# Kernel tuning notes

Hardware: AMD Instinct MI355X
Metric: run time of the kernel (lower is better)

Reference implementation:

```python
import jax, jax.numpy as jnp
import numpy as np

USER_NUM = 100000
ITEM_NUM = 100000
DIM = 64
BS = 256


def setup_inputs() -> dict:
    key = jax.random.key(0)
    k1, k2, k3, k4, k5 = jax.random.split(key, 5)
    # xavier_normal-ish scale for embeddings/linear
    user_table = jax.random.normal(k1, (USER_NUM, DIM), dtype=jnp.float32) * 0.1
    item_table = jax.random.normal(k2, (ITEM_NUM, DIM), dtype=jnp.float32) * 0.1
    cls_w = jax.random.normal(k3, (5, DIM), dtype=jnp.float32) * (2.0 / (DIM + 5)) ** 0.5
    cls_b = jnp.zeros((5,), dtype=jnp.float32)
    batch_user = jax.random.randint(k4, (BS,), 0, USER_NUM, dtype=jnp.int64)
    values = jnp.array([[1.0, 2.0, 3.0, 4.0, 5.0]], dtype=jnp.float32)
    return {
        "batch_user": batch_user,
        "user_table": user_table,
        "item_table": item_table,
        "cls_w": cls_w,
        "cls_b": cls_b,
        "values": values,
    }


def reference(batch_user, user_table, item_table, cls_w, cls_b, values):
    # forward_full_items: score every (user, item) pair.
    # Torch materializes h_ui = (u repeated) * (items tiled) of shape
    # [bs*item_num, dim]; mathematically logits = einsum over dim, so we
    # fuse the broadcasted product with the tiny Linear to avoid the
    # huge expanded intermediate while computing identical math.
    u = user_table[batch_user]                       # [bs, dim]
    # logits[b,i,c] = sum_d u[b,d] * item[i,d] * W[c,d] + b[c]
    logits = jnp.einsum('bd,id,cd->bic', u, item_table, cls_w) + cls_b  # [bs, item_num, 5]
    prob = jax.nn.softmax(logits, axis=-1)
    return jnp.sum(prob * values[0], axis=-1)        # [bs, item_num]
```

## Files before the change

### kernel.cpp

```cpp
#include <hip/hip_runtime.h>

#define I_TOTAL 100000
#define DIM 64
#define BS 256

typedef __attribute__((ext_vector_type(8))) short bf16x8;
typedef __attribute__((ext_vector_type(4))) float f32x4;

__device__ inline unsigned short f2bf(float x) {
    union { float f; unsigned u; } v; v.f = x;
    return (unsigned short)((v.u + 0x8000u) >> 16);
}

__global__ __launch_bounds__(256) void prep_M(
    const int* __restrict__ bu, const float* __restrict__ ut,
    const float* __restrict__ cw, unsigned short* __restrict__ Mbf)
{
    int idx = blockIdx.x * 256 + threadIdx.x;
    int d = (idx & 15) * 4;
    int n = idx >> 4;
    int c = n >> 8, b = n & 255;
    const float s = 1.4426950408889634f;
    float4 u = *(const float4*)(ut + (long)bu[b] * DIM + d);
    float4 w = *(const float4*)(cw + c * DIM + d);
    ushort4 r;
    r.x = f2bf(u.x * w.x * s);
    r.y = f2bf(u.y * w.y * s);
    r.z = f2bf(u.z * w.z * s);
    r.w = f2bf(u.w * w.w * s);
    *(ushort4*)(Mbf + n * DIM + d) = r;
}

__global__ __launch_bounds__(256) void conv_items(
    const float* __restrict__ item, unsigned short* __restrict__ itbf)
{
    long t = (long)blockIdx.x * 256 + threadIdx.x;
    const float4* p = (const float4*)(item + t * 8);
    float4 a = p[0], b = p[1];
    ushort4 r0, r1;
    r0.x = f2bf(a.x); r0.y = f2bf(a.y); r0.z = f2bf(a.z); r0.w = f2bf(a.w);
    r1.x = f2bf(b.x); r1.y = f2bf(b.y); r1.z = f2bf(b.z); r1.w = f2bf(b.w);
    ushort4* q = (ushort4*)(itbf + t * 8);
    q[0] = r0; q[1] = r1;
}

__global__ __launch_bounds__(256) void gemm_softmax(
    const unsigned short* __restrict__ itbf,
    const unsigned short* __restrict__ Mbf,
    const float* __restrict__ clsb, const float* __restrict__ vals,
    float* __restrict__ out)
{
    __shared__ float ldsb[4224];

    const int blk = blockIdx.x;
    const int r8 = blk & 7;
    const int q  = blk >> 3;
    const int g  = q & 15;
    const int a  = q >> 4;
    const int y  = a * 8 + r8;
    if (y >= 98) return;

    const int lane = threadIdx.x & 63;
    const int wave = threadIdx.x >> 6;
    const int col  = lane & 15;
    const int quad = lane >> 4;

    const int b_base = g * 16;
    const int i_base = y * 1024 + wave * 256;

    bf16x8 afr[5][2];
#pragma unroll
    for (int c = 0; c < 5; ++c) {
        const unsigned short* p = Mbf + (c * BS + b_base + col) * DIM + quad * 8;
        afr[c][0] = *(const bf16x8*)p;
        afr[c][1] = *(const bf16x8*)(p + 32);
    }

    const f32x4 zero = (f32x4){0.f, 0.f, 0.f, 0.f};
    const float s = 1.4426950408889634f;
    float bb[5], vv[5];
#pragma unroll
    for (int c = 0; c < 5; ++c) { bb[c] = clsb[c] * s; vv[c] = vals[c]; }

    if (y < 97) {
        float* wlds = ldsb + wave * 1056 + quad * 264 + col;
        const float* rlds = ldsb + wave * 1056 + quad * 264 + 4 * col;

        float* op[4];
#pragma unroll
        for (int k = 0; k < 4; ++k)
            op[k] = out + (size_t)(b_base + quad * 4 + k) * I_TOTAL + (i_base + 4 * col);

        const unsigned short* bp = itbf + (size_t)(i_base + col) * DIM + quad * 8;

#pragma unroll 1
        for (int t4 = 0; t4 < 4; ++t4) {
#pragma unroll
            for (int ti = 0; ti < 4; ++ti) {
                bf16x8 b0 = *(const bf16x8*)(bp + ti * 1024);
                bf16x8 b1 = *(const bf16x8*)(bp + ti * 1024 + 32);
                f32x4 acc[5];
#pragma unroll
                for (int c = 0; c < 5; ++c) {
                    acc[c] = __builtin_amdgcn_mfma_f32_16x16x32_bf16(afr[c][0], b0, zero, 0, 0, 0);
                    acc[c] = __builtin_amdgcn_mfma_f32_16x16x32_bf16(afr[c][1], b1, acc[c], 0, 0, 0);
                }
                f32x4 l[5];
#pragma unroll
                for (int c = 0; c < 5; ++c) l[c] = acc[c] + bb[c];
#pragma unroll
                for (int rr = 0; rr < 4; ++rr) {
                    float e0 = __builtin_amdgcn_exp2f(l[0][rr]);
                    float e1 = __builtin_amdgcn_exp2f(l[1][rr]);
                    float e2 = __builtin_amdgcn_exp2f(l[2][rr]);
                    float e3 = __builtin_amdgcn_exp2f(l[3][rr]);
                    float e4 = __builtin_amdgcn_exp2f(l[4][rr]);
                    float den = ((e0 + e1) + (e2 + e3)) + e4;
                    float num = e0 * vv[0];
                    num = fmaf(e1, vv[1], num);
                    num = fmaf(e2, vv[2], num);
                    num = fmaf(e3, vv[3], num);
                    num = fmaf(e4, vv[4], num);
                    wlds[rr * 64 + ti * 16] = num * __builtin_amdgcn_rcpf(den);
                }
            }
#pragma unroll
            for (int k = 0; k < 4; ++k) {
                f32x4 o4 = *(const f32x4*)(rlds + k * 64);
                *(f32x4*)op[k] = o4;
                op[k] += 64;
            }
            bp += 4 * 1024;
        }
    } else {
#pragma unroll 1
        for (int t = 0; t < 16; ++t) {
            int i  = i_base + t * 16 + col;
            int ic = i < I_TOTAL ? i : I_TOTAL - 1;
            const unsigned short* p2 = itbf + (size_t)ic * DIM + quad * 8;
            bf16x8 b0 = *(const bf16x8*)p2;
            bf16x8 b1 = *(const bf16x8*)(p2 + 32);
            f32x4 acc[5];
#pragma unroll
            for (int c = 0; c < 5; ++c) {
                acc[c] = __builtin_amdgcn_mfma_f32_16x16x32_bf16(afr[c][0], b0, zero, 0, 0, 0);
                acc[c] = __builtin_amdgcn_mfma_f32_16x16x32_bf16(afr[c][1], b1, acc[c], 0, 0, 0);
            }
            if (i < I_TOTAL) {
#pragma unroll
                for (int rr = 0; rr < 4; ++rr) {
                    float e0 = __builtin_amdgcn_exp2f(acc[0][rr] + bb[0]);
                    float e1 = __builtin_amdgcn_exp2f(acc[1][rr] + bb[1]);
                    float e2 = __builtin_amdgcn_exp2f(acc[2][rr] + bb[2]);
                    float e3 = __builtin_amdgcn_exp2f(acc[3][rr] + bb[3]);
                    float e4 = __builtin_amdgcn_exp2f(acc[4][rr] + bb[4]);
                    float den = ((e0 + e1) + (e2 + e3)) + e4;
                    float num = e0 * vv[0];
                    num = fmaf(e1, vv[1], num);
                    num = fmaf(e2, vv[2], num);
                    num = fmaf(e3, vv[3], num);
                    num = fmaf(e4, vv[4], num);
                    out[(size_t)(b_base + quad * 4 + rr) * I_TOTAL + i] =
                        num * __builtin_amdgcn_rcpf(den);
                }
            }
        }
    }
}

__global__ __launch_bounds__(256) void gemm_softmax_fb(
    const float* __restrict__ item, const unsigned short* __restrict__ Mbf,
    const float* __restrict__ clsb, const float* __restrict__ vals,
    float* __restrict__ out)
{
    const int lane = threadIdx.x & 63;
    const int wave = threadIdx.x >> 6;
    const int col  = lane & 15;
    const int quad = lane >> 4;
    const int  b_base = blockIdx.x * 16;
    const long i_wave = (long)blockIdx.y * 256 + wave * 64;

    bf16x8 afr[5][2];
#pragma unroll
    for (int c = 0; c < 5; ++c) {
        const unsigned short* p = Mbf + (c * BS + b_base + col) * DIM + quad * 8;
        afr[c][0] = *(const bf16x8*)p;
        afr[c][1] = *(const bf16x8*)(p + 32);
    }
    f32x4 acc[5][4];
#pragma unroll
    for (int c = 0; c < 5; ++c)
#pragma unroll
        for (int t = 0; t < 4; ++t) acc[c][t] = (f32x4){0.f,0.f,0.f,0.f};
#pragma unroll
    for (int t = 0; t < 4; ++t) {
        long i  = i_wave + t * 16 + col;
        long ic = (i < I_TOTAL) ? i : (I_TOTAL - 1);
        const float4* fp = (const float4*)(item + ic * DIM);
        float4 q0 = fp[2*quad], q1 = fp[2*quad+1], q2 = fp[8+2*quad], q3 = fp[8+2*quad+1];
        bf16x8 b0, b1;
        b0[0]=(short)f2bf(q0.x); b0[1]=(short)f2bf(q0.y); b0[2]=(short)f2bf(q0.z); b0[3]=(short)f2bf(q0.w);
        b0[4]=(short)f2bf(q1.x); b0[5]=(short)f2bf(q1.y); b0[6]=(short)f2bf(q1.z); b0[7]=(short)f2bf(q1.w);
        b1[0]=(short)f2bf(q2.x); b1[1]=(short)f2bf(q2.y); b1[2]=(short)f2bf(q2.z); b1[3]=(short)f2bf(q2.w);
        b1[4]=(short)f2bf(q3.x); b1[5]=(short)f2bf(q3.y); b1[6]=(short)f2bf(q3.z); b1[7]=(short)f2bf(q3.w);
#pragma unroll
        for (int c = 0; c < 5; ++c) {
            acc[c][t] = __builtin_amdgcn_mfma_f32_16x16x32_bf16(afr[c][0], b0, acc[c][t], 0, 0, 0);
            acc[c][t] = __builtin_amdgcn_mfma_f32_16x16x32_bf16(afr[c][1], b1, acc[c][t], 0, 0, 0);
        }
    }
    const float s = 1.4426950408889634f;
    float bb[5], vv[5];
#pragma unroll
    for (int c = 0; c < 5; ++c) { bb[c] = clsb[c] * s; vv[c] = vals[c]; }
#pragma unroll
    for (int t = 0; t < 4; ++t) {
        long i = i_wave + t * 16 + col;
        if (i >= I_TOTAL) continue;
#pragma unroll
        for (int r = 0; r < 4; ++r) {
            int b = b_base + quad * 4 + r;
            float num = 0.f, den = 0.f;
#pragma unroll
            for (int c = 0; c < 5; ++c) {
                float e = __builtin_amdgcn_exp2f(acc[c][t][r] + bb[c]);
                den += e; num = fmaf(e, vv[c], num);
            }
            out[(long)b * I_TOTAL + i] = num * __builtin_amdgcn_rcpf(den);
        }
    }
}

extern "C" void kernel_launch(void* const* d_in, const int* in_sizes, int n_in,
                              void* d_out, int out_size, void* d_ws, size_t ws_size,
                              hipStream_t stream) {
    const int*   bu   = (const int*)d_in[0];
    const float* ut   = (const float*)d_in[1];
    const float* it   = (const float*)d_in[2];
    const float* cw   = (const float*)d_in[3];
    const float* cb   = (const float*)d_in[4];
    const float* vals = (const float*)d_in[5];
    float* out = (float*)d_out;
    unsigned short* Mbf  = (unsigned short*)d_ws;
    unsigned short* itbf = (unsigned short*)((char*)d_ws + 163840);

    const size_t needed = 163840 + (size_t)I_TOTAL * DIM * 2;

    prep_M<<<80, 256, 0, stream>>>(bu, ut, cw, Mbf);
    if (ws_size >= needed) {
        conv_items<<<3125, 256, 0, stream>>>(it, itbf);
        gemm_softmax<<<1664, 256, 0, stream>>>(itbf, Mbf, cb, vals, out);
    } else {
        dim3 grid(16, 391);
        gemm_softmax_fb<<<grid, 256, 0, stream>>>(it, Mbf, cb, vals, out);
    }
}
```

Baseline: 177.7 us.

## Software-pipeline item-tile loads against MFMA and softmax, use nontemporal stores

After: 184.6 us. 3.9% more time.

```diff
diff --git a/kernel.cpp b/kernel.cpp
--- a/kernel.cpp
+++ b/kernel.cpp
@@ -93,44 +93,100 @@
 
         const unsigned short* bp = itbf + (size_t)(i_base + col) * DIM + quad * 8;
 
+        bf16x8 ra0 = *(const bf16x8*)(bp);
+        bf16x8 ra1 = *(const bf16x8*)(bp + 32);
+        bf16x8 ra2 = *(const bf16x8*)(bp + 1024);
+        bf16x8 ra3 = *(const bf16x8*)(bp + 1024 + 32);
+
 #pragma unroll 1
-        for (int t4 = 0; t4 < 4; ++t4) {
-#pragma unroll
-            for (int ti = 0; ti < 4; ++ti) {
-                bf16x8 b0 = *(const bf16x8*)(bp + ti * 1024);
-                bf16x8 b1 = *(const bf16x8*)(bp + ti * 1024 + 32);
-                f32x4 acc[5];
-#pragma unroll
-                for (int c = 0; c < 5; ++c) {
-                    acc[c] = __builtin_amdgcn_mfma_f32_16x16x32_bf16(afr[c][0], b0, zero, 0, 0, 0);
-                    acc[c] = __builtin_amdgcn_mfma_f32_16x16x32_bf16(afr[c][1], b1, acc[c], 0, 0, 0);
+        for (int q4 = 0; q4 < 4; ++q4) {
+            f32x4 accA[2][5];
+#pragma unroll
+            for (int c = 0; c < 5; ++c) {
+                accA[0][c] = __builtin_amdgcn_mfma_f32_16x16x32_bf16(afr[c][0], ra0, zero, 0, 0, 0);
+                accA[0][c] = __builtin_amdgcn_mfma_f32_16x16x32_bf16(afr[c][1], ra1, accA[0][c], 0, 0, 0);
+                accA[1][c] = __builtin_amdgcn_mfma_f32_16x16x32_bf16(afr[c][0], ra2, zero, 0, 0, 0);
+                accA[1][c] = __builtin_amdgcn_mfma_f32_16x16x32_bf16(afr[c][1], ra3, accA[1][c], 0, 0, 0);
+            }
+            bf16x8 rb0 = *(const bf16x8*)(bp + 2048);
+            bf16x8 rb1 = *(const bf16x8*)(bp + 2048 + 32);
+            bf16x8 rb2 = *(const bf16x8*)(bp + 3072);
+            bf16x8 rb3 = *(const bf16x8*)(bp + 3072 + 32);
+
+#pragma unroll
+            for (int t = 0; t < 2; ++t) {
+                f32x4 l0 = accA[t][0] + bb[0];
+                f32x4 l1 = accA[t][1] + bb[1];
+                f32x4 l2 = accA[t][2] + bb[2];
+                f32x4 l3 = accA[t][3] + bb[3];
+                f32x4 l4 = accA[t][4] + bb[4];
+                f32x4 e0, e1, e2, e3, e4;
+#pragma unroll
+                for (int j = 0; j < 4; ++j) {
+                    e0[j] = __builtin_amdgcn_exp2f(l0[j]);
+                    e1[j] = __builtin_amdgcn_exp2f(l1[j]);
+                    e2[j] = __builtin_amdgcn_exp2f(l2[j]);
+                    e3[j] = __builtin_amdgcn_exp2f(l3[j]);
+                    e4[j] = __builtin_amdgcn_exp2f(l4[j]);
                 }
-                f32x4 l[5];
-#pragma unroll
-                for (int c = 0; c < 5; ++c) l[c] = acc[c] + bb[c];
-#pragma unroll
-                for (int rr = 0; rr < 4; ++rr) {
-                    float e0 = __builtin_amdgcn_exp2f(l[0][rr]);
-                    float e1 = __builtin_amdgcn_exp2f(l[1][rr]);
-                    float e2 = __builtin_amdgcn_exp2f(l[2][rr]);
-                    float e3 = __builtin_amdgcn_exp2f(l[3][rr]);
-                    float e4 = __builtin_amdgcn_exp2f(l[4][rr]);
-                    float den = ((e0 + e1) + (e2 + e3)) + e4;
-                    float num = e0 * vv[0];
-                    num = fmaf(e1, vv[1], num);
-                    num = fmaf(e2, vv[2], num);
-                    num = fmaf(e3, vv[3], num);
-                    num = fmaf(e4, vv[4], num);
-                    wlds[rr * 64 + ti * 16] = num * __builtin_amdgcn_rcpf(den);
+                f32x4 den = ((e0 + e1) + (e2 + e3)) + e4;
+                f32x4 num = e0 * vv[0];
+                num += e1 * vv[1];
+                num += e2 * vv[2];
+                num += e3 * vv[3];
+                num += e4 * vv[4];
+#pragma unroll
+                for (int rr = 0; rr < 4; ++rr)
+                    wlds[rr * 64 + t * 16] = num[rr] * __builtin_amdgcn_rcpf(den[rr]);
+            }
+
+            f32x4 accB[2][5];
+#pragma unroll
+            for (int c = 0; c < 5; ++c) {
+                accB[0][c] = __builtin_amdgcn_mfma_f32_16x16x32_bf16(afr[c][0], rb0, zero, 0, 0, 0);
+                accB[0][c] = __builtin_amdgcn_mfma_f32_16x16x32_bf16(afr[c][1], rb1, accB[0][c], 0, 0, 0);
+                accB[1][c] = __builtin_amdgcn_mfma_f32_16x16x32_bf16(afr[c][0], rb2, zero, 0, 0, 0);
+                accB[1][c] = __builtin_amdgcn_mfma_f32_16x16x32_bf16(afr[c][1], rb3, accB[1][c], 0, 0, 0);
+            }
+            ra0 = *(const bf16x8*)(bp + 4096);
+            ra1 = *(const bf16x8*)(bp + 4096 + 32);
+            ra2 = *(const bf16x8*)(bp + 5120);
+            ra3 = *(const bf16x8*)(bp + 5120 + 32);
+
+#pragma unroll
+            for (int t = 0; t < 2; ++t) {
+                f32x4 l0 = accB[t][0] + bb[0];
+                f32x4 l1 = accB[t][1] + bb[1];
+                f32x4 l2 = accB[t][2] + bb[2];
+                f32x4 l3 = accB[t][3] + bb[3];
+                f32x4 l4 = accB[t][4] + bb[4];
+                f32x4 e0, e1, e2, e3, e4;
+#pragma unroll
+                for (int j = 0; j < 4; ++j) {
+                    e0[j] = __builtin_amdgcn_exp2f(l0[j]);
+                    e1[j] = __builtin_amdgcn_exp2f(l1[j]);
+                    e2[j] = __builtin_amdgcn_exp2f(l2[j]);
+                    e3[j] = __builtin_amdgcn_exp2f(l3[j]);
+                    e4[j] = __builtin_amdgcn_exp2f(l4[j]);
                 }
-            }
+                f32x4 den = ((e0 + e1) + (e2 + e3)) + e4;
+                f32x4 num = e0 * vv[0];
+                num += e1 * vv[1];
+                num += e2 * vv[2];
+                num += e3 * vv[3];
+                num += e4 * vv[4];
+#pragma unroll
+                for (int rr = 0; rr < 4; ++rr)
+                    wlds[rr * 64 + (2 + t) * 16] = num[rr] * __builtin_amdgcn_rcpf(den[rr]);
+            }
+
 #pragma unroll
             for (int k = 0; k < 4; ++k) {
                 f32x4 o4 = *(const f32x4*)(rlds + k * 64);
-                *(f32x4*)op[k] = o4;
+                __builtin_nontemporal_store(o4, (f32x4*)op[k]);
                 op[k] += 64;
             }
-            bp += 4 * 1024;
+            bp += 4096;
         }
     } else {
 #pragma unroll 1
```
